# Optimization experiments

Hardware: AMD Instinct MI355X
Metric: run time of the kernel (lower is better)

The kernel has to match this reference:

```python
import jax, jax.numpy as jnp
import numpy as np

B, C, H, W = 4, 256, 64, 64
R = 8          # rank = min(8, C//4)
G = 4          # conv groups
CG = C // G    # channels per group


def conv1x1(x, w, b):
    # x: [B,C,H,W], w: [O,C], b: [O]
    return jnp.einsum('oc,bchw->bohw', w, x) + b[None, :, None, None]


def conv1x1_grouped(x, w, b):
    # x: [B,C,H,W], w: [C, C//G] (per-output-channel slice of its group), b: [C]
    xg = x.reshape(B, G, CG, H, W)
    wg = w.reshape(G, CG, CG)  # [group, out_in_group, in_in_group]
    out = jnp.einsum('goc,bgchw->bgohw', wg, xg).reshape(B, C, H, W)
    return out + b[None, :, None, None]


def attend(q, k, v):
    # q,k: [B,R,H,W]; v: [B,C,H,W]; N = H*W
    qf = q.reshape(B, R, H * W)
    kf = k.reshape(B, R, H * W)
    vf = v.reshape(B, C, H * W)
    scores = jnp.einsum('bri,brj->bij', qf, kf)       # [B,N,N], no 1/sqrt scaling (faithful)
    attn = jax.nn.softmax(scores, axis=-1)
    out = jnp.einsum('bcm,bmn->bcn', vf, attn)        # v @ attn, contraction over query index m
    return out.reshape(B, C, H, W)


def setup_inputs():
    key = jax.random.key(0)
    ks = jax.random.split(key, 10)
    s = 0.05
    return {
        'fL': jax.random.normal(ks[0], (B, C, H, W), jnp.float32),
        'fU': jax.random.normal(ks[1], (B, C, H, W), jnp.float32),
        'qL_w': jax.random.normal(ks[2], (R, C), jnp.float32) * s,
        'qL_b': jnp.zeros((R,), jnp.float32),
        'kU_w': jax.random.normal(ks[3], (R, C), jnp.float32) * s,
        'kU_b': jnp.zeros((R,), jnp.float32),
        'vU_w': jax.random.normal(ks[4], (C, CG), jnp.float32) * s,
        'vU_b': jnp.zeros((C,), jnp.float32),
        'qU_w': jax.random.normal(ks[5], (R, C), jnp.float32) * s,
        'qU_b': jnp.zeros((R,), jnp.float32),
        'kL_w': jax.random.normal(ks[6], (R, C), jnp.float32) * s,
        'kL_b': jnp.zeros((R,), jnp.float32),
        'vL_w': jax.random.normal(ks[7], (C, CG), jnp.float32) * s,
        'vL_b': jnp.zeros((C,), jnp.float32),
        'beta': jnp.array(0.5, jnp.float32),
    }


def reference(fL, fU, qL_w, qL_b, kU_w, kU_b, vU_w, vU_b,
              qU_w, qU_b, kL_w, kL_b, vL_w, vL_b, beta):
    LU = attend(conv1x1(fL, qL_w, qL_b),
                conv1x1(fU, kU_w, kU_b),
                conv1x1_grouped(fU, vU_w, vU_b))
    UL = attend(conv1x1(fU, qU_w, qU_b),
                conv1x1(fL, kL_w, kL_b),
                conv1x1_grouped(fL, vL_w, vL_b))
    fL2 = fL + beta * LU
    fU2 = fU + beta * UL
    return (fL2, fU2)
```

## Files before the change

### kernel.cpp

```cpp
#include <hip/hip_runtime.h>

typedef float f32x4 __attribute__((ext_vector_type(4)));
typedef float f32x16 __attribute__((ext_vector_type(16)));
typedef short s16x8 __attribute__((ext_vector_type(8)));
typedef unsigned short u16;
typedef unsigned long long u64;

#define BN 4
#define CC 256
#define NN 4096

static __device__ __forceinline__ u16 f2bf(float x) {
    unsigned int u = __float_as_uint(x);
    u += 0x7FFF + ((u >> 16) & 1);
    return (u16)(u >> 16);
}

__global__ __launch_bounds__(256) void k_wtrans(
    const float* __restrict__ qLw, const float* __restrict__ kLw,
    const float* __restrict__ qUw, const float* __restrict__ kUw,
    const float* __restrict__ vUw, const float* __restrict__ vLw,
    float* __restrict__ wT, float* __restrict__ wvT)
{
    int a = blockIdx.x, t = threadIdx.x;
    const float* qw = a ? qUw : qLw;
    const float* kw = a ? kUw : kLw;
#pragma unroll
    for (int r = 0; r < 8; ++r) {
        wT[((size_t)a * 256 + t) * 16 + r]     = qw[r * 256 + t];
        wT[((size_t)a * 256 + t) * 16 + 8 + r] = kw[r * 256 + t];
    }
    const float* wv = a ? vLw : vUw;
    for (int cp = 0; cp < 64; ++cp)
        wvT[((size_t)a * 64 + cp) * 256 + t] = wv[(size_t)t * 64 + cp];
}

__global__ __launch_bounds__(512) void k_qkprep(
    const float* __restrict__ fL, const float* __restrict__ fU,
    const float* __restrict__ wT,
    const float* __restrict__ qLb, const float* __restrict__ kLb,
    const float* __restrict__ qUb, const float* __restrict__ kUb,
    u16* __restrict__ qbf, u16* __restrict__ kbf)
{
    int blk = blockIdx.x;
    int nc = blk & 31, b = (blk >> 5) & 3, src = blk >> 7;
    const float* f = src ? fU : fL;
    int qa = src, ka = 1 - src;
    int t = threadIdx.x;
    int nl = t & 127;
    int cs = __builtin_amdgcn_readfirstlane(t >> 7) * 64;
    int n = nc * 128 + nl;
    const float* fp = f + (size_t)b * 256 * NN + n;
    const float* wbase = wT + (size_t)src * 4096;

    float acc[16];
#pragma unroll
    for (int r = 0; r < 16; ++r) acc[r] = 0.f;

#pragma unroll 4
    for (int c = cs; c < cs + 64; ++c) {
        float fv = fp[(size_t)c * NN];
        const float* wr = wbase + (size_t)c * 16;
#pragma unroll
        for (int r = 0; r < 16; ++r) acc[r] += wr[r] * fv;
    }

    __shared__ float red[4][128][17];
    int cc = t >> 7;
#pragma unroll
    for (int r = 0; r < 16; ++r) red[cc][nl][r] = acc[r];
    __syncthreads();

    if (t < 128) {
        const float* bq = src ? qUb : qLb;
        const float* bk = src ? kUb : kLb;
        const float L2E = 1.4426950408889634f;
        int nn = nc * 128 + t;
        u16 pq[8], pk[8];
#pragma unroll
        for (int r = 0; r < 8; ++r) {
            float sq = red[0][t][r] + red[1][t][r] + red[2][t][r] + red[3][t][r];
            float sk = red[0][t][8+r] + red[1][t][8+r] + red[2][t][8+r] + red[3][t][8+r];
            pq[r] = f2bf((sq + bq[r]) * L2E);
            pk[r] = f2bf( sk + bk[r]);
        }
        uint4 vq, vk;
        vq.x = pq[0] | ((unsigned)pq[1] << 16); vq.y = pq[2] | ((unsigned)pq[3] << 16);
        vq.z = pq[4] | ((unsigned)pq[5] << 16); vq.w = pq[6] | ((unsigned)pq[7] << 16);
        vk.x = pk[0] | ((unsigned)pk[1] << 16); vk.y = pk[2] | ((unsigned)pk[3] << 16);
        vk.z = pk[4] | ((unsigned)pk[5] << 16); vk.w = pk[6] | ((unsigned)pk[7] << 16);
        *(uint4*)(qbf + (((size_t)qa * BN + b) * NN + nn) * 8) = vq;
        *(uint4*)(kbf + (((size_t)ka * BN + b) * NN + nn) * 8) = vk;
    }
}

__global__ __launch_bounds__(256) void k_zsum(
    const u16* __restrict__ qbf, const u16* __restrict__ kbf,
    float* __restrict__ Z)
{
    int blk = blockIdx.x;
    int mt = blk & 31, ab = blk >> 5;
    int t = threadIdx.x, l = t & 63;
    int w = __builtin_amdgcn_readfirstlane(t >> 6);
    int l31 = l & 31, g2 = l >> 5;
    int m0 = mt * 128 + w * 32;

    const u16* qab = qbf + (size_t)ab * NN * 8;
    const u16* kab = kbf + (size_t)ab * NN * 8;

    s16x8 af = *(const s16x8*)(qab + (size_t)(m0 + l31) * 8);
    if (g2) af = (s16x8)0;

    auto ldb = [&](int i) -> s16x8 {
        s16x8 r = *(const s16x8*)(kab + (size_t)(i * 32 + l31) * 8);
        return g2 ? (s16x8)0 : r;
    };

    float zp[16];
#pragma unroll
    for (int r = 0; r < 16; ++r) zp[r] = 0.f;

    s16x8 b0 = ldb(0), b1 = ldb(1);
#pragma unroll 1
    for (int i = 0; i < 128; ++i) {
        int nx = i + 2 < 127 ? i + 2 : 127;
        s16x8 bn = ldb(nx);
        f32x16 s = __builtin_amdgcn_mfma_f32_32x32x16_bf16(af, b0, (f32x16)0.f, 0, 0, 0);
#pragma unroll
        for (int r = 0; r < 16; ++r) zp[r] += __builtin_exp2f(s[r]);
        b0 = b1; b1 = bn;
    }

#pragma unroll
    for (int r = 0; r < 16; ++r) {
        float v = zp[r];
#pragma unroll
        for (int d = 1; d < 32; d <<= 1) v += __shfl_xor(v, d, 64);
        zp[r] = v;
    }
    if (l31 == 0) {
#pragma unroll
        for (int r = 0; r < 16; ++r) {
            int m = m0 + (r & 3) + 8 * (r >> 2) + 4 * g2;
            Z[(size_t)ab * NN + m] = zp[r];
        }
    }
}

__global__ __launch_bounds__(256) void k_vprep(
    const float* __restrict__ fL, const float* __restrict__ fU,
    const float* __restrict__ wvT,
    const float* __restrict__ vUb, const float* __restrict__ vLb,
    const float* __restrict__ Z, u16* __restrict__ vpt)
{
    int blk = blockIdx.x;
    int mc = blk & 31, g = (blk >> 5) & 3, ab = blk >> 7;
    int a = ab >> 2, b = ab & 3;
    const float* f    = a ? fL : fU;
    const float* bias = a ? vLb : vUb;
    int t = threadIdx.x, l = t & 63;
    int wu = __builtin_amdgcn_readfirstlane(t >> 6);
    int m0 = mc * 128 + l * 2;

    const float* fg = f + ((size_t)b * 256 + g * 64) * NN + m0;
    const float* wq = wvT + (size_t)a * 16384 + g * 64 + wu * 16;

    float acc[16][2];
#pragma unroll
    for (int j = 0; j < 16; ++j) { acc[j][0] = 0.f; acc[j][1] = 0.f; }

    for (int cp = 0; cp < 64; ++cp) {
        float2 fv = *(const float2*)(fg + (size_t)cp * NN);
        const float* wr = wq + (size_t)cp * 256;
        float4 w0 = *(const float4*)(wr);
        float4 w1 = *(const float4*)(wr + 4);
        float4 w2 = *(const float4*)(wr + 8);
        float4 w3 = *(const float4*)(wr + 12);
        float wv[16] = {w0.x,w0.y,w0.z,w0.w, w1.x,w1.y,w1.z,w1.w,
                        w2.x,w2.y,w2.z,w2.w, w3.x,w3.y,w3.z,w3.w};
#pragma unroll
        for (int j = 0; j < 16; ++j) {
            acc[j][0] += wv[j] * fv.x;
            acc[j][1] += wv[j] * fv.y;
        }
    }

    float2 z = *(const float2*)(Z + (size_t)ab * NN + m0);
    float zr0 = 1.f / z.x, zr1 = 1.f / z.y;
    int mt = m0 >> 5, mi = m0 & 31;
    u16* vpo = vpt + (((size_t)ab * 128 + mt) * 256 + g * 64 + wu * 16) * 32 + mi;
#pragma unroll
    for (int j = 0; j < 16; ++j) {
        float bj = bias[g * 64 + wu * 16 + j];
        unsigned pk = (unsigned)f2bf((acc[j][0] + bj) * zr0) |
                      ((unsigned)f2bf((acc[j][1] + bj) * zr1) << 16);
        *(unsigned*)(vpo + (size_t)j * 32) = pk;
    }
}

__global__ __launch_bounds__(512, 4) void k_main(
    const float* __restrict__ fL, const float* __restrict__ fU,
    const u16* __restrict__ qbf, const u16* __restrict__ kbf,
    const u16* __restrict__ vpt, const float* __restrict__ beta_p,
    float* __restrict__ out)
{
    int blk = blockIdx.x;
    int ab = blk & 7, nt = blk >> 3;
    int a = ab >> 2, b = ab & 3;
    int n0 = nt * 64;
    int t = threadIdx.x, l = t & 63;
    int w = __builtin_amdgcn_readfirstlane(t >> 6);
    int c15 = l & 15, g = l >> 4;
    int ng = w & 3;
    int mh = w >> 2;
    int swz = (c15 & 7) << 4;

    __shared__ u16 ebuf[2][64][64];

    auto eptr = [&](int p, int n, int mbyte) -> char* {
        return ((char*)ebuf) + (p << 13) + (n << 7) + (mbyte ^ swz);
    };

    const u16* qab = qbf + (size_t)ab * NN * 8;
    const u16* kab = kbf + (size_t)ab * NN * 8;

    s16x8 bkf = *(const s16x8*)(kab + (size_t)(n0 + ng * 16 + c15) * 8);
    if (g) bkf = (s16x8)0;

    const u16* apb = vpt + (size_t)ab * (128ull * 8192)
                   + (size_t)(w * 32 + c15) * 32 + g * 8;

    f32x4 acc[2][4];
#pragma unroll
    for (int i = 0; i < 2; ++i)
#pragma unroll
        for (int j = 0; j < 4; ++j) acc[i][j] = (f32x4)0.f;

    auto qld = [&](int win, int mq2) -> s16x8 {
        s16x8 r = *(const s16x8*)(qab + (size_t)(win * 64 + (mh * 2 + mq2) * 16 + c15) * 8);
        return g ? (s16x8)0 : r;
    };

    auto egen = [&](int pbuf, const s16x8& q0, const s16x8& q1) {
#pragma unroll
        for (int mq2 = 0; mq2 < 2; ++mq2) {
            f32x4 s = __builtin_amdgcn_mfma_f32_16x16x32_bf16(
                mq2 ? q1 : q0, bkf, (f32x4)0.f, 0, 0, 0);
            float e0 = __builtin_exp2f(s[0]);
            float e1 = __builtin_exp2f(s[1]);
            float e2 = __builtin_exp2f(s[2]);
            float e3 = __builtin_exp2f(s[3]);
            unsigned lo, hi;
            asm("v_cvt_pk_bf16_f32 %0, %1, %2" : "=v"(lo) : "v"(e0), "v"(e1));
            asm("v_cvt_pk_bf16_f32 %0, %1, %2" : "=v"(hi) : "v"(e2), "v"(e3));
            uint2 pk; pk.x = lo; pk.y = hi;
            *(uint2*)eptr(pbuf, ng * 16 + c15, (mh * 2 + mq2) * 32 + g * 8) = pk;
        }
    };

    auto step = [&](int P, int kwin,
                    s16x8 (&aC)[2][2], s16x8 (&aN)[2][2],
                    s16x8 (&qC)[2], s16x8 (&qN)[2], bool doeg) {
        int kn = kwin + 1 < 63 ? kwin + 1 : 63;
        const u16* apn = apb + (size_t)(2 * kn) * 8192;
#pragma unroll
        for (int cf = 0; cf < 2; ++cf) {
            aN[cf][0] = *(const s16x8*)(apn + cf * 512);
            aN[cf][1] = *(const s16x8*)(apn + 8192 + cf * 512);
        }
        int kq = kwin + 2 < 63 ? kwin + 2 : 63;
        qN[0] = qld(kq, 0);
        qN[1] = qld(kq, 1);

        s16x8 bf[4];
#pragma unroll
        for (int nf = 0; nf < 4; ++nf)
            bf[nf] = *(const s16x8*)eptr(P, nf * 16 + c15, g * 16);
        if (doeg) egen(P ^ 1, qC[0], qC[1]);
        __builtin_amdgcn_s_setprio(1);
#pragma unroll
        for (int cf = 0; cf < 2; ++cf)
#pragma unroll
            for (int nf = 0; nf < 4; ++nf)
                acc[cf][nf] = __builtin_amdgcn_mfma_f32_16x16x32_bf16(
                    aC[cf][0], bf[nf], acc[cf][nf], 0, 0, 0);
        __builtin_amdgcn_s_setprio(0);
#pragma unroll
        for (int nf = 0; nf < 4; ++nf)
            bf[nf] = *(const s16x8*)eptr(P, nf * 16 + c15, 64 + g * 16);
        __builtin_amdgcn_s_setprio(1);
#pragma unroll
        for (int cf = 0; cf < 2; ++cf)
#pragma unroll
            for (int nf = 0; nf < 4; ++nf)
                acc[cf][nf] = __builtin_amdgcn_mfma_f32_16x16x32_bf16(
                    aC[cf][1], bf[nf], acc[cf][nf], 0, 0, 0);
        __builtin_amdgcn_s_setprio(0);
        asm volatile("s_waitcnt lgkmcnt(0)\n\ts_barrier" ::: "memory");
    };

    {
        s16x8 z0 = qld(0, 0), z1 = qld(0, 1);
        egen(0, z0, z1);
    }
    s16x8 qA[2], qB[2];
    qA[0] = qld(1, 0); qA[1] = qld(1, 1);
    s16x8 afA[2][2], afB[2][2];
#pragma unroll
    for (int cf = 0; cf < 2; ++cf) {
        afA[cf][0] = *(const s16x8*)(apb + cf * 512);
        afA[cf][1] = *(const s16x8*)(apb + 8192 + cf * 512);
    }
    __syncthreads();

#pragma unroll 1
    for (int k2 = 0; k2 < 32; ++k2) {
        step(0, 2 * k2,     afA, afB, qA, qB, true);
        step(1, 2 * k2 + 1, afB, afA, qB, qA, k2 < 31);
    }

    float beta = beta_p[0];
    const float* base = a ? fU : fL;
    float* op = out + (size_t)a * ((size_t)BN * CC * NN);
#pragma unroll
    for (int cf = 0; cf < 2; ++cf)
#pragma unroll
        for (int nf = 0; nf < 4; ++nf)
#pragma unroll
            for (int r = 0; r < 4; ++r) {
                int c = w * 32 + cf * 16 + g * 4 + r;
                int n = n0 + nf * 16 + c15;
                size_t idx = ((size_t)b * CC + c) * NN + n;
                op[idx] = base[idx] + beta * acc[cf][nf][r];
            }
}

extern "C" void kernel_launch(void* const* d_in, const int* in_sizes, int n_in,
                              void* d_out, int out_size, void* d_ws, size_t ws_size,
                              hipStream_t stream) {
    const float* fL  = (const float*)d_in[0];
    const float* fU  = (const float*)d_in[1];
    const float* qLw = (const float*)d_in[2];
    const float* qLb = (const float*)d_in[3];
    const float* kUw = (const float*)d_in[4];
    const float* kUb = (const float*)d_in[5];
    const float* vUw = (const float*)d_in[6];
    const float* vUb = (const float*)d_in[7];
    const float* qUw = (const float*)d_in[8];
    const float* qUb = (const float*)d_in[9];
    const float* kLw = (const float*)d_in[10];
    const float* kLb = (const float*)d_in[11];
    const float* vLw = (const float*)d_in[12];
    const float* vLb = (const float*)d_in[13];
    const float* beta = (const float*)d_in[14];

    char* ws = (char*)d_ws;
    float* wT  = (float*)(ws);
    float* wvT = (float*)(ws + 32768);
    u16*   qbf = (u16*)  (ws + 163840);
    u16*   kbf = (u16*)  (ws + 688128);
    float* Z   = (float*)(ws + 1212416);
    u16*   vpt = (u16*)  (ws + 1343488);
    float* out = (float*)d_out;

    k_wtrans<<<2, 256, 0, stream>>>(qLw, kLw, qUw, kUw, vUw, vLw, wT, wvT);
    k_qkprep<<<256, 512, 0, stream>>>(fL, fU, wT, qLb, kLb, qUb, kUb, qbf, kbf);
    k_zsum<<<256, 256, 0, stream>>>(qbf, kbf, Z);
    k_vprep<<<1024, 256, 0, stream>>>(fL, fU, wvT, vUb, vLb, Z, vpt);
    k_main<<<512, 512, 0, stream>>>(fL, fU, qbf, kbf, vpt, beta, out);
}
```

Before: 176.7 us.

## Retile attention main kernel to 128 keys by 128 channels per block

The main attention kernel changes its block tile from 64 query columns by all 256 channels to 128 columns by a 128-channel half. The channel dimension is now split across two blocks. Each wave computes its own 16-row strip of the exp tile and accumulates a 64x32 output patch, so each A fragment feeds two MFMAs and each exp fragment feeds four. The aim is to spread the per-block exp generation cost and V loads differently and to raise MFMA reuse per register. In exchange the score exponentials are recomputed twice, once per channel half, and LDS usage doubles.

```diff
diff --git a/kernel.cpp b/kernel.cpp
--- a/kernel.cpp
+++ b/kernel.cpp
@@ -205,131 +205,115 @@
     float* __restrict__ out)
 {
     int blk = blockIdx.x;
-    int ab = blk & 7, nt = blk >> 3;
+    int ab = blk & 7, ch = (blk >> 3) & 1, nt = blk >> 4;
     int a = ab >> 2, b = ab & 3;
-    int n0 = nt * 64;
+    int n0 = nt * 128, c0 = ch * 128;
     int t = threadIdx.x, l = t & 63;
     int w = __builtin_amdgcn_readfirstlane(t >> 6);
     int c15 = l & 15, g = l >> 4;
-    int ng = w & 3;
-    int mh = w >> 2;
+    int cs = w & 1, nh = w >> 1;
     int swz = (c15 & 7) << 4;
 
-    __shared__ u16 ebuf[2][64][64];
+    __shared__ u16 ebuf[2][128][64];
 
     auto eptr = [&](int p, int n, int mbyte) -> char* {
-        return ((char*)ebuf) + (p << 13) + (n << 7) + (mbyte ^ swz);
+        return ((char*)ebuf) + (p << 14) + (n << 7) + (mbyte ^ swz);
     };
 
     const u16* qab = qbf + (size_t)ab * NN * 8;
     const u16* kab = kbf + (size_t)ab * NN * 8;
 
-    s16x8 bkf = *(const s16x8*)(kab + (size_t)(n0 + ng * 16 + c15) * 8);
+    s16x8 bkf = *(const s16x8*)(kab + (size_t)(n0 + w * 16 + c15) * 8);
     if (g) bkf = (s16x8)0;
 
-    const u16* apb = vpt + (size_t)ab * (128ull * 8192)
-                   + (size_t)(w * 32 + c15) * 32 + g * 8;
-
-    f32x4 acc[2][4];
-#pragma unroll
-    for (int i = 0; i < 2; ++i)
-#pragma unroll
-        for (int j = 0; j < 4; ++j) acc[i][j] = (f32x4)0.f;
-
-    auto qld = [&](int win, int mq2) -> s16x8 {
-        s16x8 r = *(const s16x8*)(qab + (size_t)(win * 64 + (mh * 2 + mq2) * 16 + c15) * 8);
-        return g ? (s16x8)0 : r;
+    f32x4 acc[4][2];
+#pragma unroll
+    for (int i = 0; i < 4; ++i) { acc[i][0] = (f32x4)0.f; acc[i][1] = (f32x4)0.f; }
+
+    auto epiece = [&](int pbuf, int mq, s16x8 qv) {
+        f32x4 s = __builtin_amdgcn_mfma_f32_16x16x32_bf16(qv, bkf, (f32x4)0.f, 0, 0, 0);
+        float e0 = __builtin_exp2f(s[0]);
+        float e1 = __builtin_exp2f(s[1]);
+        float e2 = __builtin_exp2f(s[2]);
+        float e3 = __builtin_exp2f(s[3]);
+        unsigned lo, hi;
+        asm("v_cvt_pk_bf16_f32 %0, %1, %2" : "=v"(lo) : "v"(e0), "v"(e1));
+        asm("v_cvt_pk_bf16_f32 %0, %1, %2" : "=v"(hi) : "v"(e2), "v"(e3));
+        uint2 pk; pk.x = lo; pk.y = hi;
+        *(uint2*)eptr(pbuf, w * 16 + c15, mq * 32 + g * 8) = pk;
     };
 
-    auto egen = [&](int pbuf, const s16x8& q0, const s16x8& q1) {
-#pragma unroll
-        for (int mq2 = 0; mq2 < 2; ++mq2) {
-            f32x4 s = __builtin_amdgcn_mfma_f32_16x16x32_bf16(
-                mq2 ? q1 : q0, bkf, (f32x4)0.f, 0, 0, 0);
-            float e0 = __builtin_exp2f(s[0]);
-            float e1 = __builtin_exp2f(s[1]);
-            float e2 = __builtin_exp2f(s[2]);
-            float e3 = __builtin_exp2f(s[3]);
-            unsigned lo, hi;
-            asm("v_cvt_pk_bf16_f32 %0, %1, %2" : "=v"(lo) : "v"(e0), "v"(e1));
-            asm("v_cvt_pk_bf16_f32 %0, %1, %2" : "=v"(hi) : "v"(e2), "v"(e3));
-            uint2 pk; pk.x = lo; pk.y = hi;
-            *(uint2*)eptr(pbuf, ng * 16 + c15, (mh * 2 + mq2) * 32 + g * 8) = pk;
+    {
+        const u16* qp = qab + (size_t)c15 * 8;
+#pragma unroll
+        for (int mq = 0; mq < 4; ++mq) {
+            s16x8 qv = *(const s16x8*)(qp + (size_t)mq * 128);
+            if (g) qv = (s16x8)0;
+            epiece(0, mq, qv);
         }
+    }
+
+    const u16* qpt = qab + (size_t)(64 + c15) * 8;
+    s16x8 qA[2], qB[2];
+    qA[0] = *(const s16x8*)(qpt);
+    qA[1] = *(const s16x8*)(qpt + 128);
+    if (g) { qA[0] = (s16x8)0; qA[1] = (s16x8)0; }
+    qpt += 256;
+
+    const u16* apt = vpt + (size_t)ab * (128ull * 8192)
+                   + (size_t)(c0 + cs * 64 + c15) * 32 + g * 8;
+    s16x8 aA[4], aB[4];
+#pragma unroll
+    for (int cf = 0; cf < 4; ++cf) aA[cf] = *(const s16x8*)(apt + cf * 512);
+    apt += 8192;
+
+    __syncthreads();
+
+    auto half = [&](int P, int kc, s16x8 (&aC)[4], s16x8 (&aN)[4],
+                    s16x8 (&qC)[2], s16x8 (&qN)[2], bool doeg, bool adv) {
+#pragma unroll
+        for (int cf = 0; cf < 4; ++cf) aN[cf] = *(const s16x8*)(apt + cf * 512);
+        apt += adv ? 8192 : 0;
+        s16x8 q0 = *(const s16x8*)(qpt);
+        s16x8 q1 = *(const s16x8*)(qpt + 128);
+        qpt += 256;
+        s16x8 bf0 = *(const s16x8*)eptr(P, nh * 32 + c15,      kc * 64 + g * 16);
+        s16x8 bf1 = *(const s16x8*)eptr(P, nh * 32 + 16 + c15, kc * 64 + g * 16);
+        if (doeg) { epiece(P ^ 1, kc * 2, qC[0]); epiece(P ^ 1, kc * 2 + 1, qC[1]); }
+        if (g) { q0 = (s16x8)0; q1 = (s16x8)0; }
+        qN[0] = q0; qN[1] = q1;
+        __builtin_amdgcn_s_setprio(1);
+#pragma unroll
+        for (int cf = 0; cf < 4; ++cf)
+            acc[cf][0] = __builtin_amdgcn_mfma_f32_16x16x32_bf16(aC[cf], bf0, acc[cf][0], 0, 0, 0);
+#pragma unroll
+        for (int cf = 0; cf < 4; ++cf)
+            acc[cf][1] = __builtin_amdgcn_mfma_f32_16x16x32_bf16(aC[cf], bf1, acc[cf][1], 0, 0, 0);
+        __builtin_amdgcn_s_setprio(0);
     };
-
-    auto step = [&](int P, int kwin,
-                    s16x8 (&aC)[2][2], s16x8 (&aN)[2][2],
-                    s16x8 (&qC)[2], s16x8 (&qN)[2], bool doeg) {
-        int kn = kwin + 1 < 63 ? kwin + 1 : 63;
-        const u16* apn = apb + (size_t)(2 * kn) * 8192;
-#pragma unroll
-        for (int cf = 0; cf < 2; ++cf) {
-            aN[cf][0] = *(const s16x8*)(apn + cf * 512);
-            aN[cf][1] = *(const s16x8*)(apn + 8192 + cf * 512);
-        }
-        int kq = kwin + 2 < 63 ? kwin + 2 : 63;
-        qN[0] = qld(kq, 0);
-        qN[1] = qld(kq, 1);
-
-        s16x8 bf[4];
-#pragma unroll
-        for (int nf = 0; nf < 4; ++nf)
-            bf[nf] = *(const s16x8*)eptr(P, nf * 16 + c15, g * 16);
-        if (doeg) egen(P ^ 1, qC[0], qC[1]);
-        __builtin_amdgcn_s_setprio(1);
-#pragma unroll
-        for (int cf = 0; cf < 2; ++cf)
-#pragma unroll
-            for (int nf = 0; nf < 4; ++nf)
-                acc[cf][nf] = __builtin_amdgcn_mfma_f32_16x16x32_bf16(
-                    aC[cf][0], bf[nf], acc[cf][nf], 0, 0, 0);
-        __builtin_amdgcn_s_setprio(0);
-#pragma unroll
-        for (int nf = 0; nf < 4; ++nf)
-            bf[nf] = *(const s16x8*)eptr(P, nf * 16 + c15, 64 + g * 16);
-        __builtin_amdgcn_s_setprio(1);
-#pragma unroll
-        for (int cf = 0; cf < 2; ++cf)
-#pragma unroll
-            for (int nf = 0; nf < 4; ++nf)
-                acc[cf][nf] = __builtin_amdgcn_mfma_f32_16x16x32_bf16(
-                    aC[cf][1], bf[nf], acc[cf][nf], 0, 0, 0);
-        __builtin_amdgcn_s_setprio(0);
-        asm volatile("s_waitcnt lgkmcnt(0)\n\ts_barrier" ::: "memory");
-    };
-
-    {
-        s16x8 z0 = qld(0, 0), z1 = qld(0, 1);
-        egen(0, z0, z1);
-    }
-    s16x8 qA[2], qB[2];
-    qA[0] = qld(1, 0); qA[1] = qld(1, 1);
-    s16x8 afA[2][2], afB[2][2];
-#pragma unroll
-    for (int cf = 0; cf < 2; ++cf) {
-        afA[cf][0] = *(const s16x8*)(apb + cf * 512);
-        afA[cf][1] = *(const s16x8*)(apb + 8192 + cf * 512);
-    }
-    __syncthreads();
 
 #pragma unroll 1
     for (int k2 = 0; k2 < 32; ++k2) {
-        step(0, 2 * k2,     afA, afB, qA, qB, true);
-        step(1, 2 * k2 + 1, afB, afA, qB, qA, k2 < 31);
+        bool last = (k2 == 31);
+        half(0, 0, aA, aB, qA, qB, true, true);
+        half(0, 1, aB, aA, qB, qA, true, true);
+        asm volatile("s_waitcnt lgkmcnt(0)\n\ts_barrier" ::: "memory");
+        half(1, 0, aA, aB, qA, qB, !last, !last);
+        half(1, 1, aB, aA, qB, qA, !last, !last);
+        asm volatile("s_waitcnt lgkmcnt(0)\n\ts_barrier" ::: "memory");
     }
 
     float beta = beta_p[0];
     const float* base = a ? fU : fL;
     float* op = out + (size_t)a * ((size_t)BN * CC * NN);
 #pragma unroll
-    for (int cf = 0; cf < 2; ++cf)
-#pragma unroll
-        for (int nf = 0; nf < 4; ++nf)
+    for (int cf = 0; cf < 4; ++cf)
+#pragma unroll
+        for (int nf = 0; nf < 2; ++nf)
 #pragma unroll
             for (int r = 0; r < 4; ++r) {
-                int c = w * 32 + cf * 16 + g * 4 + r;
-                int n = n0 + nf * 16 + c15;
+                int c = c0 + cs * 64 + cf * 16 + g * 4 + r;
+                int n = n0 + nh * 32 + nf * 16 + c15;
                 size_t idx = ((size_t)b * CC + c) * NN + n;
                 op[idx] = base[idx] + beta * acc[cf][nf][r];
             }
```

New measurement: 242.7 us. 37.4% more time.

## Fuse q/k projection into v-projection pass and apply softmax normalizer in main kernel

Applied to the files above, without the earlier changes.

The q/k 1x1 projections are now computed in the same pass over the input features as the grouped v projection. Each block writes partial per-group q/k sums to a new fp32 scratch buffer, and a small reduction kernel adds the biases and converts them to bf16. Because of this, the input tensors are read once instead of twice. V no longer depends on the softmax denominator, so the zsum kernel stores reciprocal normalizers and the main kernel multiplies each exp2 by the per-query reciprocal. This adds an extra 8MB scratch round trip, one more launch, and extra loads and multiplies in the main kernel's inner loop.

```diff
diff --git a/kernel.cpp b/kernel.cpp
--- a/kernel.cpp
+++ b/kernel.cpp
@@ -35,139 +35,32 @@
         wvT[((size_t)a * 64 + cp) * 256 + t] = wv[(size_t)t * 64 + cp];
 }
 
-__global__ __launch_bounds__(512) void k_qkprep(
+__global__ __launch_bounds__(256) void k_prep(
     const float* __restrict__ fL, const float* __restrict__ fU,
-    const float* __restrict__ wT,
-    const float* __restrict__ qLb, const float* __restrict__ kLb,
-    const float* __restrict__ qUb, const float* __restrict__ kUb,
-    u16* __restrict__ qbf, u16* __restrict__ kbf)
-{
-    int blk = blockIdx.x;
-    int nc = blk & 31, b = (blk >> 5) & 3, src = blk >> 7;
-    const float* f = src ? fU : fL;
-    int qa = src, ka = 1 - src;
-    int t = threadIdx.x;
-    int nl = t & 127;
-    int cs = __builtin_amdgcn_readfirstlane(t >> 7) * 64;
-    int n = nc * 128 + nl;
-    const float* fp = f + (size_t)b * 256 * NN + n;
-    const float* wbase = wT + (size_t)src * 4096;
-
-    float acc[16];
-#pragma unroll
-    for (int r = 0; r < 16; ++r) acc[r] = 0.f;
-
-#pragma unroll 4
-    for (int c = cs; c < cs + 64; ++c) {
-        float fv = fp[(size_t)c * NN];
-        const float* wr = wbase + (size_t)c * 16;
-#pragma unroll
-        for (int r = 0; r < 16; ++r) acc[r] += wr[r] * fv;
-    }
-
-    __shared__ float red[4][128][17];
-    int cc = t >> 7;
-#pragma unroll
-    for (int r = 0; r < 16; ++r) red[cc][nl][r] = acc[r];
-    __syncthreads();
-
-    if (t < 128) {
-        const float* bq = src ? qUb : qLb;
-        const float* bk = src ? kUb : kLb;
-        const float L2E = 1.4426950408889634f;
-        int nn = nc * 128 + t;
-        u16 pq[8], pk[8];
-#pragma unroll
-        for (int r = 0; r < 8; ++r) {
-            float sq = red[0][t][r] + red[1][t][r] + red[2][t][r] + red[3][t][r];
-            float sk = red[0][t][8+r] + red[1][t][8+r] + red[2][t][8+r] + red[3][t][8+r];
-            pq[r] = f2bf((sq + bq[r]) * L2E);
-            pk[r] = f2bf( sk + bk[r]);
-        }
-        uint4 vq, vk;
-        vq.x = pq[0] | ((unsigned)pq[1] << 16); vq.y = pq[2] | ((unsigned)pq[3] << 16);
-        vq.z = pq[4] | ((unsigned)pq[5] << 16); vq.w = pq[6] | ((unsigned)pq[7] << 16);
-        vk.x = pk[0] | ((unsigned)pk[1] << 16); vk.y = pk[2] | ((unsigned)pk[3] << 16);
-        vk.z = pk[4] | ((unsigned)pk[5] << 16); vk.w = pk[6] | ((unsigned)pk[7] << 16);
-        *(uint4*)(qbf + (((size_t)qa * BN + b) * NN + nn) * 8) = vq;
-        *(uint4*)(kbf + (((size_t)ka * BN + b) * NN + nn) * 8) = vk;
-    }
-}
-
-__global__ __launch_bounds__(256) void k_zsum(
-    const u16* __restrict__ qbf, const u16* __restrict__ kbf,
-    float* __restrict__ Z)
-{
-    int blk = blockIdx.x;
-    int mt = blk & 31, ab = blk >> 5;
-    int t = threadIdx.x, l = t & 63;
-    int w = __builtin_amdgcn_readfirstlane(t >> 6);
-    int l31 = l & 31, g2 = l >> 5;
-    int m0 = mt * 128 + w * 32;
-
-    const u16* qab = qbf + (size_t)ab * NN * 8;
-    const u16* kab = kbf + (size_t)ab * NN * 8;
-
-    s16x8 af = *(const s16x8*)(qab + (size_t)(m0 + l31) * 8);
-    if (g2) af = (s16x8)0;
-
-    auto ldb = [&](int i) -> s16x8 {
-        s16x8 r = *(const s16x8*)(kab + (size_t)(i * 32 + l31) * 8);
-        return g2 ? (s16x8)0 : r;
-    };
-
-    float zp[16];
-#pragma unroll
-    for (int r = 0; r < 16; ++r) zp[r] = 0.f;
-
-    s16x8 b0 = ldb(0), b1 = ldb(1);
-#pragma unroll 1
-    for (int i = 0; i < 128; ++i) {
-        int nx = i + 2 < 127 ? i + 2 : 127;
-        s16x8 bn = ldb(nx);
-        f32x16 s = __builtin_amdgcn_mfma_f32_32x32x16_bf16(af, b0, (f32x16)0.f, 0, 0, 0);
-#pragma unroll
-        for (int r = 0; r < 16; ++r) zp[r] += __builtin_exp2f(s[r]);
-        b0 = b1; b1 = bn;
-    }
-
-#pragma unroll
-    for (int r = 0; r < 16; ++r) {
-        float v = zp[r];
-#pragma unroll
-        for (int d = 1; d < 32; d <<= 1) v += __shfl_xor(v, d, 64);
-        zp[r] = v;
-    }
-    if (l31 == 0) {
-#pragma unroll
-        for (int r = 0; r < 16; ++r) {
-            int m = m0 + (r & 3) + 8 * (r >> 2) + 4 * g2;
-            Z[(size_t)ab * NN + m] = zp[r];
-        }
-    }
-}
-
-__global__ __launch_bounds__(256) void k_vprep(
-    const float* __restrict__ fL, const float* __restrict__ fU,
-    const float* __restrict__ wvT,
+    const float* __restrict__ wvT, const float* __restrict__ wT,
     const float* __restrict__ vUb, const float* __restrict__ vLb,
-    const float* __restrict__ Z, u16* __restrict__ vpt)
+    u16* __restrict__ vpt, float* __restrict__ qkp)
 {
     int blk = blockIdx.x;
     int mc = blk & 31, g = (blk >> 5) & 3, ab = blk >> 7;
     int a = ab >> 2, b = ab & 3;
     const float* f    = a ? fL : fU;
     const float* bias = a ? vLb : vUb;
+    int src = 1 - a;
     int t = threadIdx.x, l = t & 63;
     int wu = __builtin_amdgcn_readfirstlane(t >> 6);
     int m0 = mc * 128 + l * 2;
 
     const float* fg = f + ((size_t)b * 256 + g * 64) * NN + m0;
     const float* wq = wvT + (size_t)a * 16384 + g * 64 + wu * 16;
+    const float* wk = wT + (size_t)src * 4096 + (size_t)(g * 64) * 16 + wu * 4;
 
     float acc[16][2];
+    float qk[4][2];
 #pragma unroll
     for (int j = 0; j < 16; ++j) { acc[j][0] = 0.f; acc[j][1] = 0.f; }
+#pragma unroll
+    for (int r = 0; r < 4; ++r) { qk[r][0] = 0.f; qk[r][1] = 0.f; }
 
     for (int cp = 0; cp < 64; ++cp) {
         float2 fv = *(const float2*)(fg + (size_t)cp * NN);
@@ -176,6 +69,7 @@
         float4 w1 = *(const float4*)(wr + 4);
         float4 w2 = *(const float4*)(wr + 8);
         float4 w3 = *(const float4*)(wr + 12);
+        float4 vv = *(const float4*)(wk + (size_t)cp * 16);
         float wv[16] = {w0.x,w0.y,w0.z,w0.w, w1.x,w1.y,w1.z,w1.w,
                         w2.x,w2.y,w2.z,w2.w, w3.x,w3.y,w3.z,w3.w};
 #pragma unroll
@@ -183,24 +77,127 @@
             acc[j][0] += wv[j] * fv.x;
             acc[j][1] += wv[j] * fv.y;
         }
-    }
-
-    float2 z = *(const float2*)(Z + (size_t)ab * NN + m0);
-    float zr0 = 1.f / z.x, zr1 = 1.f / z.y;
+        float qv[4] = {vv.x, vv.y, vv.z, vv.w};
+#pragma unroll
+        for (int r = 0; r < 4; ++r) {
+            qk[r][0] += qv[r] * fv.x;
+            qk[r][1] += qv[r] * fv.y;
+        }
+    }
+
     int mt = m0 >> 5, mi = m0 & 31;
     u16* vpo = vpt + (((size_t)ab * 128 + mt) * 256 + g * 64 + wu * 16) * 32 + mi;
 #pragma unroll
     for (int j = 0; j < 16; ++j) {
         float bj = bias[g * 64 + wu * 16 + j];
-        unsigned pk = (unsigned)f2bf((acc[j][0] + bj) * zr0) |
-                      ((unsigned)f2bf((acc[j][1] + bj) * zr1) << 16);
+        unsigned pk = (unsigned)f2bf(acc[j][0] + bj) |
+                      ((unsigned)f2bf(acc[j][1] + bj) << 16);
         *(unsigned*)(vpo + (size_t)j * 32) = pk;
+    }
+    float* qo = qkp + ((size_t)((src * 4 + b) * 4 + g) * 16 + wu * 4) * NN + m0;
+#pragma unroll
+    for (int rr = 0; rr < 4; ++rr) {
+        float2 pv; pv.x = qk[rr][0]; pv.y = qk[rr][1];
+        *(float2*)(qo + (size_t)rr * NN) = pv;
+    }
+}
+
+__global__ __launch_bounds__(256) void k_qkred(
+    const float* __restrict__ qkp,
+    const float* __restrict__ qLb, const float* __restrict__ kLb,
+    const float* __restrict__ qUb, const float* __restrict__ kUb,
+    u16* __restrict__ qbf, u16* __restrict__ kbf)
+{
+    int gm = blockIdx.x * 256 + threadIdx.x;
+    int sb = gm >> 12, m = gm & 4095;
+    int src = sb >> 2, b = sb & 3;
+    const float* base = qkp + (size_t)sb * 64 * NN + m;
+
+    float s[16];
+#pragma unroll
+    for (int r = 0; r < 16; ++r) s[r] = 0.f;
+#pragma unroll
+    for (int g = 0; g < 4; ++g)
+#pragma unroll
+        for (int r = 0; r < 16; ++r)
+            s[r] += base[(size_t)(g * 16 + r) * NN];
+
+    const float* bq = src ? qUb : qLb;
+    const float* bk = src ? kUb : kLb;
+    const float L2E = 1.4426950408889634f;
+    u16 pq[8], pk[8];
+#pragma unroll
+    for (int r = 0; r < 8; ++r) {
+        pq[r] = f2bf((s[r] + bq[r]) * L2E);
+        pk[r] = f2bf( s[8 + r] + bk[r]);
+    }
+    uint4 vq, vk;
+    vq.x = pq[0] | ((unsigned)pq[1] << 16); vq.y = pq[2] | ((unsigned)pq[3] << 16);
+    vq.z = pq[4] | ((unsigned)pq[5] << 16); vq.w = pq[6] | ((unsigned)pq[7] << 16);
+    vk.x = pk[0] | ((unsigned)pk[1] << 16); vk.y = pk[2] | ((unsigned)pk[3] << 16);
+    vk.z = pk[4] | ((unsigned)pk[5] << 16); vk.w = pk[6] | ((unsigned)pk[7] << 16);
+    int qa = src, ka = 1 - src;
+    *(uint4*)(qbf + (((size_t)qa * BN + b) * NN + m) * 8) = vq;
+    *(uint4*)(kbf + (((size_t)ka * BN + b) * NN + m) * 8) = vk;
+}
+
+__global__ __launch_bounds__(256) void k_zsum(
+    const u16* __restrict__ qbf, const u16* __restrict__ kbf,
+    float* __restrict__ Zi)
+{
+    int blk = blockIdx.x;
+    int mt = blk & 31, ab = blk >> 5;
+    int t = threadIdx.x, l = t & 63;
+    int w = __builtin_amdgcn_readfirstlane(t >> 6);
+    int l31 = l & 31, g2 = l >> 5;
+    int m0 = mt * 128 + w * 32;
+
+    const u16* qab = qbf + (size_t)ab * NN * 8;
+    const u16* kab = kbf + (size_t)ab * NN * 8;
+
+    s16x8 af = *(const s16x8*)(qab + (size_t)(m0 + l31) * 8);
+    if (g2) af = (s16x8)0;
+
+    auto ldb = [&](int i) -> s16x8 {
+        s16x8 r = *(const s16x8*)(kab + (size_t)(i * 32 + l31) * 8);
+        return g2 ? (s16x8)0 : r;
+    };
+
+    float zp[16];
+#pragma unroll
+    for (int r = 0; r < 16; ++r) zp[r] = 0.f;
+
+    s16x8 b0 = ldb(0), b1 = ldb(1);
+#pragma unroll 1
+    for (int i = 0; i < 128; ++i) {
+        int nx = i + 2 < 127 ? i + 2 : 127;
+        s16x8 bn = ldb(nx);
+        f32x16 s = __builtin_amdgcn_mfma_f32_32x32x16_bf16(af, b0, (f32x16)0.f, 0, 0, 0);
+#pragma unroll
+        for (int r = 0; r < 16; ++r) zp[r] += __builtin_exp2f(s[r]);
+        b0 = b1; b1 = bn;
+    }
+
+#pragma unroll
+    for (int r = 0; r < 16; ++r) {
+        float v = zp[r];
+#pragma unroll
+        for (int d = 1; d < 32; d <<= 1) v += __shfl_xor(v, d, 64);
+        zp[r] = v;
+    }
+    if (l31 == 0) {
+#pragma unroll
+        for (int r = 0; r < 16; ++r) {
+            int m = m0 + (r & 3) + 8 * (r >> 2) + 4 * g2;
+            Zi[(size_t)ab * NN + m] = 1.0f / zp[r];
+        }
     }
 }
 
 __global__ __launch_bounds__(512, 4) void k_main(
     const float* __restrict__ fL, const float* __restrict__ fU,
     const u16* __restrict__ qbf, const u16* __restrict__ kbf,
+    const float* __restrict__ Zi,
     const u16* __restrict__ vpt, const float* __restrict__ beta_p,
     float* __restrict__ out)
 {
@@ -223,6 +220,7 @@
 
     const u16* qab = qbf + (size_t)ab * NN * 8;
     const u16* kab = kbf + (size_t)ab * NN * 8;
+    const float* Ziab = Zi + (size_t)ab * NN;
 
     s16x8 bkf = *(const s16x8*)(kab + (size_t)(n0 + ng * 16 + c15) * 8);
     if (g) bkf = (s16x8)0;
@@ -240,16 +238,21 @@
         s16x8 r = *(const s16x8*)(qab + (size_t)(win * 64 + (mh * 2 + mq2) * 16 + c15) * 8);
         return g ? (s16x8)0 : r;
     };
-
-    auto egen = [&](int pbuf, const s16x8& q0, const s16x8& q1) {
+    auto zld = [&](int win, int mq2) -> float4 {
+        return *(const float4*)(Ziab + win * 64 + (mh * 2 + mq2) * 16 + g * 4);
+    };
+
+    auto egen = [&](int pbuf, const s16x8& q0, const s16x8& q1,
+                    const float4& z0, const float4& z1) {
 #pragma unroll
         for (int mq2 = 0; mq2 < 2; ++mq2) {
             f32x4 s = __builtin_amdgcn_mfma_f32_16x16x32_bf16(
                 mq2 ? q1 : q0, bkf, (f32x4)0.f, 0, 0, 0);
-            float e0 = __builtin_exp2f(s[0]);
-            float e1 = __builtin_exp2f(s[1]);
-            float e2 = __builtin_exp2f(s[2]);
-            float e3 = __builtin_exp2f(s[3]);
+            float4 zz = mq2 ? z1 : z0;
+            float e0 = __builtin_exp2f(s[0]) * zz.x;
+            float e1 = __builtin_exp2f(s[1]) * zz.y;
+            float e2 = __builtin_exp2f(s[2]) * zz.z;
+            float e3 = __builtin_exp2f(s[3]) * zz.w;
             unsigned lo, hi;
             asm("v_cvt_pk_bf16_f32 %0, %1, %2" : "=v"(lo) : "v"(e0), "v"(e1));
             asm("v_cvt_pk_bf16_f32 %0, %1, %2" : "=v"(hi) : "v"(e2), "v"(e3));
@@ -260,7 +263,8 @@
 
     auto step = [&](int P, int kwin,
                     s16x8 (&aC)[2][2], s16x8 (&aN)[2][2],
-                    s16x8 (&qC)[2], s16x8 (&qN)[2], bool doeg) {
+                    s16x8 (&qC)[2], s16x8 (&qN)[2],
+                    float4 (&zC)[2], float4 (&zN)[2], bool doeg) {
         int kn = kwin + 1 < 63 ? kwin + 1 : 63;
         const u16* apn = apb + (size_t)(2 * kn) * 8192;
 #pragma unroll
@@ -271,12 +275,14 @@
         int kq = kwin + 2 < 63 ? kwin + 2 : 63;
         qN[0] = qld(kq, 0);
         qN[1] = qld(kq, 1);
+        zN[0] = zld(kq, 0);
+        zN[1] = zld(kq, 1);
 
         s16x8 bf[4];
 #pragma unroll
         for (int nf = 0; nf < 4; ++nf)
             bf[nf] = *(const s16x8*)eptr(P, nf * 16 + c15, g * 16);
-        if (doeg) egen(P ^ 1, qC[0], qC[1]);
+        if (doeg) egen(P ^ 1, qC[0], qC[1], zC[0], zC[1]);
         __builtin_amdgcn_s_setprio(1);
 #pragma unroll
         for (int cf = 0; cf < 2; ++cf)
@@ -301,10 +307,13 @@
 
     {
         s16x8 z0 = qld(0, 0), z1 = qld(0, 1);
-        egen(0, z0, z1);
+        float4 y0 = zld(0, 0), y1 = zld(0, 1);
+        egen(0, z0, z1, y0, y1);
     }
     s16x8 qA[2], qB[2];
+    float4 zA[2], zB[2];
     qA[0] = qld(1, 0); qA[1] = qld(1, 1);
+    zA[0] = zld(1, 0); zA[1] = zld(1, 1);
     s16x8 afA[2][2], afB[2][2];
 #pragma unroll
     for (int cf = 0; cf < 2; ++cf) {
@@ -315,8 +324,8 @@
 
 #pragma unroll 1
     for (int k2 = 0; k2 < 32; ++k2) {
-        step(0, 2 * k2,     afA, afB, qA, qB, true);
-        step(1, 2 * k2 + 1, afB, afA, qB, qA, k2 < 31);
+        step(0, 2 * k2,     afA, afB, qA, qB, zA, zB, true);
+        step(1, 2 * k2 + 1, afB, afA, qB, qA, zB, zA, k2 < 31);
     }
 
     float beta = beta_p[0];
@@ -357,15 +366,16 @@
     char* ws = (char*)d_ws;
     float* wT  = (float*)(ws);
     float* wvT = (float*)(ws + 32768);
-    u16*   qbf = (u16*)  (ws + 163840);
-    u16*   kbf = (u16*)  (ws + 688128);
-    float* Z   = (float*)(ws + 1212416);
-    u16*   vpt = (u16*)  (ws + 1343488);
+    float* qkp = (float*)(ws + 163840);
+    u16*   qbf = (u16*)  (ws + 8552448);
+    u16*   kbf = (u16*)  (ws + 9076736);
+    float* Zi  = (float*)(ws + 9601024);
+    u16*   vpt = (u16*)  (ws + 9732096);
     float* out = (float*)d_out;
 
     k_wtrans<<<2, 256, 0, stream>>>(qLw, kLw, qUw, kUw, vUw, vLw, wT, wvT);
-    k_qkprep<<<256, 512, 0, stream>>>(fL, fU, wT, qLb, kLb, qUb, kUb, qbf, kbf);
-    k_zsum<<<256, 256, 0, stream>>>(qbf, kbf, Z);
-    k_vprep<<<1024, 256, 0, stream>>>(fL, fU, wvT, vUb, vLb, Z, vpt);
-    k_main<<<512, 512, 0, stream>>>(fL, fU, qbf, kbf, vpt, beta, out);
-}
+    k_prep<<<1024, 256, 0, stream>>>(fL, fU, wvT, wT, vUb, vLb, vpt, qkp);
+    k_qkred<<<128, 256, 0, stream>>>(qkp, qLb, kLb, qUb, kUb, qbf, kbf);
+    k_zsum<<<256, 256, 0, stream>>>(qbf, kbf, Zi);
+    k_main<<<512, 512, 0, stream>>>(fL, fU, qbf, kbf, Zi, vpt, beta, out);
+}
```

New measurement: 180.3 us. +2.1%, slower.
